# Performance work log

Hardware: AMD Instinct MI355X
Metric: run time of the kernel (lower is better)

The kernel has to match this reference:

```python
import jax, jax.numpy as jnp
import numpy as np

HIDDEN = 512
TEMPERATURE = float(np.sqrt(HIDDEN))  # scaled-dot temperature
BATCH = 64


def _build_weights(attn_weight, N, K):
    """Vectorized version of get_attn_weight: (S,S,H) with S = N*K+1.
    Regions: 0=same_sample, 1=same_class, 2=diff_class, 3=support->query,
    4=query->support, 5=query->query. Replicates the torch overwrite order."""
    S = N * K + 1
    NK = N * K
    i = jnp.arange(S)[:, None]
    j = jnp.arange(S)[None, :]
    idx = jnp.full((S, S), 2, dtype=jnp.int32)                      # w_diff_class
    idx = jnp.where((i // K) == (j // K), 1, idx)                   # w_same_class
    idx = jnp.where((i < NK) & (j == NK), 3, idx)                   # w_stoquery
    idx = jnp.where(i == j, 0, idx)                                 # w_same_sample (diag)
    idx = jnp.where((i == NK) & (j < NK), 4, idx)                   # w_querytos
    idx = jnp.where((i == NK) & (j == NK), 5, idx)                  # w_query
    return attn_weight[idx]  # (S, S, H)


def setup_inputs() -> dict:
    key = jax.random.key(0)
    kq, kk, kv, kw = jax.random.split(key, 4)
    N, K = 10, 10
    S = N * K + 1  # 101
    q = jax.random.normal(kq, (BATCH, S, HIDDEN), dtype=jnp.float32)
    k = jax.random.normal(kk, (BATCH, S, HIDDEN), dtype=jnp.float32)
    v = jax.random.normal(kv, (BATCH, S, HIDDEN), dtype=jnp.float32)
    bound = float(np.sqrt(6 / 2))
    attn_weight = jax.random.uniform(kw, (6, HIDDEN), dtype=jnp.float32,
                                     minval=-bound, maxval=bound)
    return {"q": q, "k": k, "v": v, "attn_weight": attn_weight, "N": N, "K": K}


def reference(q, k, v, attn_weight, N, K):
    # attn[b,i,j] = softmax_j(q.k^T / temperature)
    scores = jnp.einsum("bih,bjh->bij", q, k) / TEMPERATURE
    attn = jax.nn.softmax(scores, axis=2)  # dropout p=0 (eval) -> identity
    weights = _build_weights(attn_weight, N, K)  # (S,S,H)
    # out[b,i,h] = sum_j attn[b,i,j] * weights[i,j,h] * v[b,j,h]
    out = jnp.einsum("bij,ijh,bjh->bih", attn, weights, v)
    return out, attn
```

## Files before the change

### kernel.cpp

```cpp
#include <hip/hip_runtime.h>
#include <math.h>
#include <stdint.h>

#define BATCH 64
#define SEQ   101
#define HID   512
#define NKQ   100
#define KCLS  10
#define INV_TEMP 0.04419417382415922f
#define SPAD  128

typedef short bf16x8 __attribute__((ext_vector_type(8)));
typedef float f32x4  __attribute__((ext_vector_type(4)));

__device__ inline void split_bf16(float x, short& hi, short& lo) {
    uint32_t u = __builtin_bit_cast(uint32_t, x);
    hi = (short)(u >> 16);
    float hf = __builtin_bit_cast(float, u & 0xFFFF0000u);
    float l  = x - hf;
    lo = (short)(__builtin_bit_cast(uint32_t, l) >> 16);
}

__global__ __launch_bounds__(512, 4)
void fused_attn(const float* __restrict__ q, const float* __restrict__ k,
                const float* __restrict__ v, const float* __restrict__ aw,
                float* __restrict__ out, float* __restrict__ attn) {
    __shared__ float sc[16][132];
    __shared__ short ah_s[16][136];
    __shared__ short al_s[16][136];
    __shared__ short mh_s[16][136];

    const int b   = blockIdx.x & 63;
    const int i0  = (blockIdx.x >> 6) * 16;
    const int tid = threadIdx.x;
    const int wv  = tid >> 6, lane = tid & 63;
    const int m   = lane & 15;
    const int kq  = (lane >> 4) * 8;
    const int rq  = (lane >> 4) * 4;

    const float* qb = q + (size_t)b * SEQ * HID;
    const float* kb = k + (size_t)b * SEQ * HID;
    const float* vb = v + (size_t)b * SEQ * HID;

    {
        const int j0w = wv * 16;
        const int qrow = i0 + m;
        const int krow = j0w + m;
        f32x4 acc = {};
        for (int ks = 0; ks < HID; ks += 32) {
            float x[8];
            bf16x8 qh, ql, kh, kl;
            if (qrow < SEQ) {
                float4 u0 = *(const float4*)(qb + (size_t)qrow * HID + ks + kq);
                float4 u1 = *(const float4*)(qb + (size_t)qrow * HID + ks + kq + 4);
                x[0]=u0.x; x[1]=u0.y; x[2]=u0.z; x[3]=u0.w;
                x[4]=u1.x; x[5]=u1.y; x[6]=u1.z; x[7]=u1.w;
            } else {
                #pragma unroll
                for (int e = 0; e < 8; ++e) x[e] = 0.f;
            }
            #pragma unroll
            for (int e = 0; e < 8; ++e) { short h,l; split_bf16(x[e],h,l); qh[e]=h; ql[e]=l; }
            if (krow < SEQ) {
                float4 u0 = *(const float4*)(kb + (size_t)krow * HID + ks + kq);
                float4 u1 = *(const float4*)(kb + (size_t)krow * HID + ks + kq + 4);
                x[0]=u0.x; x[1]=u0.y; x[2]=u0.z; x[3]=u0.w;
                x[4]=u1.x; x[5]=u1.y; x[6]=u1.z; x[7]=u1.w;
            } else {
                #pragma unroll
                for (int e = 0; e < 8; ++e) x[e] = 0.f;
            }
            #pragma unroll
            for (int e = 0; e < 8; ++e) { short h,l; split_bf16(x[e],h,l); kh[e]=h; kl[e]=l; }
            acc = __builtin_amdgcn_mfma_f32_16x16x32_bf16(qh, kh, acc, 0, 0, 0);
            acc = __builtin_amdgcn_mfma_f32_16x16x32_bf16(qh, kl, acc, 0, 0, 0);
            acc = __builtin_amdgcn_mfma_f32_16x16x32_bf16(ql, kh, acc, 0, 0, 0);
        }
        #pragma unroll
        for (int r = 0; r < 4; ++r)
            sc[rq + r][j0w + m] = acc[r];
    }
    __syncthreads();

    {
        const int row = tid >> 5, t32 = tid & 31;
        const int gi  = i0 + row;
        float mx = -1e30f;
        for (int j = t32; j < SEQ; j += 32) {
            float s = sc[row][j] * INV_TEMP;
            sc[row][j] = s;
            mx = fmaxf(mx, s);
        }
        #pragma unroll
        for (int off = 1; off < 32; off <<= 1) mx = fmaxf(mx, __shfl_xor(mx, off));
        float sum = 0.f;
        for (int j = t32; j < SEQ; j += 32) {
            float e = __expf(sc[row][j] - mx);
            sc[row][j] = e;
            sum += e;
        }
        #pragma unroll
        for (int off = 1; off < 32; off <<= 1) sum += __shfl_xor(sum, off);
        const float inv = 1.f / sum;
        const int ci = gi / KCLS;
        float* arow = attn + ((size_t)b * SEQ + gi) * SEQ;
        for (int j = t32; j < SEQ; j += 32) {
            float a = sc[row][j] * inv;
            sc[row][j] = a;
            if (gi < SEQ) arow[j] = a;
            short h, l; split_bf16(a, h, l);
            ah_s[row][j] = h; al_s[row][j] = l;
            mh_s[row][j] = ((j / KCLS) == ci) ? h : (short)0;
        }
        for (int j = SEQ + t32; j < 136; j += 32) {
            ah_s[row][j] = 0; al_s[row][j] = 0; mh_s[row][j] = 0;
        }
    }
    __syncthreads();

    const int hw = wv * 64;
    f32x4 T[4] = {}, U[4] = {};
    for (int ks = 0; ks < SPAD; ks += 32) {
        const bf16x8 Ah = *(const bf16x8*)&ah_s[m][ks + kq];
        const bf16x8 Al = *(const bf16x8*)&al_s[m][ks + kq];
        const bf16x8 Mh = *(const bf16x8*)&mh_s[m][ks + kq];
        #pragma unroll
        for (int ht = 0; ht < 4; ++ht) {
            const int h = hw + ht * 16 + m;
            float x[8];
            #pragma unroll
            for (int e = 0; e < 8; ++e) {
                const int j = ks + kq + e;
                x[e] = (j < SEQ) ? vb[(size_t)j * HID + h] : 0.f;
            }
            bf16x8 Bh, Bl;
            #pragma unroll
            for (int e = 0; e < 8; ++e) { short hh,ll; split_bf16(x[e],hh,ll); Bh[e]=hh; Bl[e]=ll; }
            T[ht] = __builtin_amdgcn_mfma_f32_16x16x32_bf16(Ah, Bh, T[ht], 0, 0, 0);
            T[ht] = __builtin_amdgcn_mfma_f32_16x16x32_bf16(Ah, Bl, T[ht], 0, 0, 0);
            T[ht] = __builtin_amdgcn_mfma_f32_16x16x32_bf16(Al, Bh, T[ht], 0, 0, 0);
            U[ht] = __builtin_amdgcn_mfma_f32_16x16x32_bf16(Mh, Bh, U[ht], 0, 0, 0);
        }
    }

    #pragma unroll
    for (int ht = 0; ht < 4; ++ht) {
        const int h = hw + ht * 16 + m;
        const float w0 = aw[0 * HID + h], w1 = aw[1 * HID + h], w2 = aw[2 * HID + h];
        const float w3 = aw[3 * HID + h], w4 = aw[4 * HID + h], w5 = aw[5 * HID + h];
        const float vN = vb[(size_t)NKQ * HID + h];
        #pragma unroll
        for (int r = 0; r < 4; ++r) {
            const int il = rq + r;
            const int i  = i0 + il;
            if (i >= SEQ) continue;
            const float t = T[ht][r], u = U[ht][r];
            const float aiN = sc[il][NKQ];
            float o;
            if (i < NKQ) {
                const float aii = sc[il][i];
                const float vi  = vb[(size_t)i * HID + h];
                o = w2 * t + (w1 - w2) * u + (w0 - w1) * aii * vi + (w3 - w2) * aiN * vN;
            } else {
                o = w4 * t + (w5 - w4) * aiN * vN;
            }
            out[((size_t)b * SEQ + i) * HID + h] = o;
        }
    }
}

extern "C" void kernel_launch(void* const* d_in, const int* in_sizes, int n_in,
                              void* d_out, int out_size, void* d_ws, size_t ws_size,
                              hipStream_t stream) {
    const float* q  = (const float*)d_in[0];
    const float* k  = (const float*)d_in[1];
    const float* v  = (const float*)d_in[2];
    const float* aw = (const float*)d_in[3];
    float* out  = (float*)d_out;
    float* attn = out + (size_t)BATCH * SEQ * HID;

    fused_attn<<<dim3(448), dim3(512), 0, stream>>>(q, k, v, aw, out, attn);
}
```

Before: 121.0 us.

## Precompute bf16 hi/lo splits in prep kernel and split hidden dim across blocks

New measurement: 185.2 us. 53.1% more time.

```diff
diff --git a/kernel.cpp b/kernel.cpp
--- a/kernel.cpp
+++ b/kernel.cpp
@@ -8,10 +8,12 @@
 #define NKQ   100
 #define KCLS  10
 #define INV_TEMP 0.04419417382415922f
-#define SPAD  128
 
 typedef short bf16x8 __attribute__((ext_vector_type(8)));
 typedef float f32x4  __attribute__((ext_vector_type(4)));
+
+#define QK_PLANE ((size_t)BATCH * SEQ * HID)
+#define VT_PLANE ((size_t)BATCH * HID * 128)
 
 __device__ inline void split_bf16(float x, short& hi, short& lo) {
     uint32_t u = __builtin_bit_cast(uint32_t, x);
@@ -21,60 +23,97 @@
     lo = (short)(__builtin_bit_cast(uint32_t, l) >> 16);
 }
 
+__global__ __launch_bounds__(256)
+void prep_bf16(const float* __restrict__ q, const float* __restrict__ k,
+               const float* __restrict__ v,
+               short* __restrict__ qh, short* __restrict__ ql,
+               short* __restrict__ kh, short* __restrict__ kl,
+               short* __restrict__ vh, short* __restrict__ vl) {
+    const int tid = threadIdx.x;
+    if (blockIdx.x < 256) {
+        __shared__ float tile[SEQ][132];
+        const int b = blockIdx.x & 63, hc = (blockIdx.x >> 6) * 128;
+        const float* vb = v + (size_t)b * SEQ * HID + hc;
+        for (int f = tid; f < SEQ * 32; f += 256) {
+            int r = f >> 5, c = (f & 31) << 2;
+            *(float4*)&tile[r][c] = *(const float4*)(vb + (size_t)r * HID + c);
+        }
+        __syncthreads();
+        const int hl = tid >> 1;
+        const int j0 = (tid & 1) * 64;
+        const size_t ro = ((size_t)b * HID + hc + hl) * 128 + j0;
+        for (int jj = 0; jj < 64; jj += 4) {
+            short4 hv, lv;
+            int j = j0 + jj;
+            split_bf16(j + 0 < SEQ ? tile[j + 0][hl] : 0.f, hv.x, lv.x);
+            split_bf16(j + 1 < SEQ ? tile[j + 1][hl] : 0.f, hv.y, lv.y);
+            split_bf16(j + 2 < SEQ ? tile[j + 2][hl] : 0.f, hv.z, lv.z);
+            split_bf16(j + 3 < SEQ ? tile[j + 3][hl] : 0.f, hv.w, lv.w);
+            *(short4*)(vh + ro + jj) = hv;
+            *(short4*)(vl + ro + jj) = lv;
+        }
+    } else {
+        const size_t per = QK_PLANE / 4;
+        for (size_t f = (size_t)(blockIdx.x - 256) * 256 + tid;
+             f < 2 * per; f += (size_t)512 * 256) {
+            size_t e = f;
+            const float* src; short *dh, *dl;
+            if (e < per) { src = q; dh = qh; dl = ql; }
+            else         { e -= per; src = k; dh = kh; dl = kl; }
+            float4 x = ((const float4*)src)[e];
+            short4 hv, lv;
+            split_bf16(x.x, hv.x, lv.x);
+            split_bf16(x.y, hv.y, lv.y);
+            split_bf16(x.z, hv.z, lv.z);
+            split_bf16(x.w, hv.w, lv.w);
+            *(short4*)(dh + e * 4) = hv;
+            *(short4*)(dl + e * 4) = lv;
+        }
+    }
+}
+
 __global__ __launch_bounds__(512, 4)
-void fused_attn(const float* __restrict__ q, const float* __restrict__ k,
-                const float* __restrict__ v, const float* __restrict__ aw,
+void fused_attn(const float* __restrict__ v, const float* __restrict__ aw,
+                const short* __restrict__ qh, const short* __restrict__ ql,
+                const short* __restrict__ kh, const short* __restrict__ kl,
+                const short* __restrict__ vh, const short* __restrict__ vl,
                 float* __restrict__ out, float* __restrict__ attn) {
     __shared__ float sc[16][132];
     __shared__ short ah_s[16][136];
     __shared__ short al_s[16][136];
     __shared__ short mh_s[16][136];
 
-    const int b   = blockIdx.x & 63;
-    const int i0  = (blockIdx.x >> 6) * 16;
+    const int id  = blockIdx.x;
+    const int b   = id & 63;
+    const int rr  = id >> 6;
+    const int it  = rr % 7, hg = rr / 7;
+    const int i0  = it * 16;
     const int tid = threadIdx.x;
     const int wv  = tid >> 6, lane = tid & 63;
     const int m   = lane & 15;
     const int kq  = (lane >> 4) * 8;
     const int rq  = (lane >> 4) * 4;
 
-    const float* qb = q + (size_t)b * SEQ * HID;
-    const float* kb = k + (size_t)b * SEQ * HID;
     const float* vb = v + (size_t)b * SEQ * HID;
 
     {
         const int j0w = wv * 16;
-        const int qrow = i0 + m;
-        const int krow = j0w + m;
+        int qrow = i0 + m;  if (qrow > NKQ) qrow = NKQ;
+        int krow = j0w + m; if (krow > NKQ) krow = NKQ;
+        const short* qhr = qh + ((size_t)b * SEQ + qrow) * HID + kq;
+        const short* qlr = ql + ((size_t)b * SEQ + qrow) * HID + kq;
+        const short* khr = kh + ((size_t)b * SEQ + krow) * HID + kq;
+        const short* klr = kl + ((size_t)b * SEQ + krow) * HID + kq;
         f32x4 acc = {};
+        #pragma unroll 4
         for (int ks = 0; ks < HID; ks += 32) {
-            float x[8];
-            bf16x8 qh, ql, kh, kl;
-            if (qrow < SEQ) {
-                float4 u0 = *(const float4*)(qb + (size_t)qrow * HID + ks + kq);
-                float4 u1 = *(const float4*)(qb + (size_t)qrow * HID + ks + kq + 4);
-                x[0]=u0.x; x[1]=u0.y; x[2]=u0.z; x[3]=u0.w;
-                x[4]=u1.x; x[5]=u1.y; x[6]=u1.z; x[7]=u1.w;
-            } else {
-                #pragma unroll
-                for (int e = 0; e < 8; ++e) x[e] = 0.f;
-            }
-            #pragma unroll
-            for (int e = 0; e < 8; ++e) { short h,l; split_bf16(x[e],h,l); qh[e]=h; ql[e]=l; }
-            if (krow < SEQ) {
-                float4 u0 = *(const float4*)(kb + (size_t)krow * HID + ks + kq);
-                float4 u1 = *(const float4*)(kb + (size_t)krow * HID + ks + kq + 4);
-                x[0]=u0.x; x[1]=u0.y; x[2]=u0.z; x[3]=u0.w;
-                x[4]=u1.x; x[5]=u1.y; x[6]=u1.z; x[7]=u1.w;
-            } else {
-                #pragma unroll
-                for (int e = 0; e < 8; ++e) x[e] = 0.f;
-            }
-            #pragma unroll
-            for (int e = 0; e < 8; ++e) { short h,l; split_bf16(x[e],h,l); kh[e]=h; kl[e]=l; }
-            acc = __builtin_amdgcn_mfma_f32_16x16x32_bf16(qh, kh, acc, 0, 0, 0);
-            acc = __builtin_amdgcn_mfma_f32_16x16x32_bf16(qh, kl, acc, 0, 0, 0);
-            acc = __builtin_amdgcn_mfma_f32_16x16x32_bf16(ql, kh, acc, 0, 0, 0);
+            bf16x8 aH = *(const bf16x8*)(qhr + ks);
+            bf16x8 aL = *(const bf16x8*)(qlr + ks);
+            bf16x8 bH = *(const bf16x8*)(khr + ks);
+            bf16x8 bL = *(const bf16x8*)(klr + ks);
+            acc = __builtin_amdgcn_mfma_f32_16x16x32_bf16(aH, bH, acc, 0, 0, 0);
+            acc = __builtin_amdgcn_mfma_f32_16x16x32_bf16(aH, bL, acc, 0, 0, 0);
+            acc = __builtin_amdgcn_mfma_f32_16x16x32_bf16(aL, bH, acc, 0, 0, 0);
         }
         #pragma unroll
         for (int r = 0; r < 4; ++r)
@@ -107,7 +146,7 @@
         for (int j = t32; j < SEQ; j += 32) {
             float a = sc[row][j] * inv;
             sc[row][j] = a;
-            if (gi < SEQ) arow[j] = a;
+            if (hg == 0 && gi < SEQ) arow[j] = a;
             short h, l; split_bf16(a, h, l);
             ah_s[row][j] = h; al_s[row][j] = l;
             mh_s[row][j] = ((j / KCLS) == ci) ? h : (short)0;
@@ -118,24 +157,19 @@
     }
     __syncthreads();
 
-    const int hw = wv * 64;
-    f32x4 T[4] = {}, U[4] = {};
-    for (int ks = 0; ks < SPAD; ks += 32) {
+    const int hb = hg * 256 + wv * 32;
+    f32x4 T[2] = {}, U[2] = {};
+    #pragma unroll
+    for (int ks = 0; ks < 128; ks += 32) {
         const bf16x8 Ah = *(const bf16x8*)&ah_s[m][ks + kq];
         const bf16x8 Al = *(const bf16x8*)&al_s[m][ks + kq];
         const bf16x8 Mh = *(const bf16x8*)&mh_s[m][ks + kq];
         #pragma unroll
-        for (int ht = 0; ht < 4; ++ht) {
-            const int h = hw + ht * 16 + m;
-            float x[8];
-            #pragma unroll
-            for (int e = 0; e < 8; ++e) {
-                const int j = ks + kq + e;
-                x[e] = (j < SEQ) ? vb[(size_t)j * HID + h] : 0.f;
-            }
-            bf16x8 Bh, Bl;
-            #pragma unroll
-            for (int e = 0; e < 8; ++e) { short hh,ll; split_bf16(x[e],hh,ll); Bh[e]=hh; Bl[e]=ll; }
+        for (int ht = 0; ht < 2; ++ht) {
+            const int h = hb + ht * 16 + m;
+            const size_t vo = ((size_t)b * HID + h) * 128 + ks + kq;
+            const bf16x8 Bh = *(const bf16x8*)(vh + vo);
+            const bf16x8 Bl = *(const bf16x8*)(vl + vo);
             T[ht] = __builtin_amdgcn_mfma_f32_16x16x32_bf16(Ah, Bh, T[ht], 0, 0, 0);
             T[ht] = __builtin_amdgcn_mfma_f32_16x16x32_bf16(Ah, Bl, T[ht], 0, 0, 0);
             T[ht] = __builtin_amdgcn_mfma_f32_16x16x32_bf16(Al, Bh, T[ht], 0, 0, 0);
@@ -144,8 +178,8 @@
     }
 
     #pragma unroll
-    for (int ht = 0; ht < 4; ++ht) {
-        const int h = hw + ht * 16 + m;
+    for (int ht = 0; ht < 2; ++ht) {
+        const int h = hb + ht * 16 + m;
         const float w0 = aw[0 * HID + h], w1 = aw[1 * HID + h], w2 = aw[2 * HID + h];
         const float w3 = aw[3 * HID + h], w4 = aw[4 * HID + h], w5 = aw[5 * HID + h];
         const float vN = vb[(size_t)NKQ * HID + h];
@@ -179,5 +213,14 @@
     float* out  = (float*)d_out;
     float* attn = out + (size_t)BATCH * SEQ * HID;
 
-    fused_attn<<<dim3(448), dim3(512), 0, stream>>>(q, k, v, aw, out, attn);
-}
+    short* qh = (short*)d_ws;
+    short* ql = qh + QK_PLANE;
+    short* kh = ql + QK_PLANE;
+    short* kl = kh + QK_PLANE;
+    short* vh = kl + QK_PLANE;
+    short* vl = vh + VT_PLANE;
+
+    prep_bf16<<<dim3(768), dim3(256), 0, stream>>>(q, k, v, qh, ql, kh, kl, vh, vl);
+    fused_attn<<<dim3(896), dim3(512), 0, stream>>>(v, aw, qh, ql, kh, kl, vh, vl,
+                                                    out, attn);
+}
```

## Split fused attention into QK-softmax and PV kernels with LDS-staged V

Applied to the files above, without the earlier changes.

Measured after the change: 126.5 us. 4.6% more time.

```diff
diff --git a/kernel.cpp b/kernel.cpp
--- a/kernel.cpp
+++ b/kernel.cpp
@@ -8,7 +8,6 @@
 #define NKQ   100
 #define KCLS  10
 #define INV_TEMP 0.04419417382415922f
-#define SPAD  128
 
 typedef short bf16x8 __attribute__((ext_vector_type(8)));
 typedef float f32x4  __attribute__((ext_vector_type(4)));
@@ -22,14 +21,9 @@
 }
 
 __global__ __launch_bounds__(512, 4)
-void fused_attn(const float* __restrict__ q, const float* __restrict__ k,
-                const float* __restrict__ v, const float* __restrict__ aw,
-                float* __restrict__ out, float* __restrict__ attn) {
+void qk_softmax(const float* __restrict__ q, const float* __restrict__ k,
+                float* __restrict__ attn, float* __restrict__ apad) {
     __shared__ float sc[16][132];
-    __shared__ short ah_s[16][136];
-    __shared__ short al_s[16][136];
-    __shared__ short mh_s[16][136];
-
     const int b   = blockIdx.x & 63;
     const int i0  = (blockIdx.x >> 6) * 16;
     const int tid = threadIdx.x;
@@ -40,41 +34,30 @@
 
     const float* qb = q + (size_t)b * SEQ * HID;
     const float* kb = k + (size_t)b * SEQ * HID;
-    const float* vb = v + (size_t)b * SEQ * HID;
 
     {
         const int j0w = wv * 16;
-        const int qrow = i0 + m;
-        const int krow = j0w + m;
+        int qrow = i0 + m;  if (qrow > NKQ) qrow = NKQ;
+        int krow = j0w + m; if (krow > NKQ) krow = NKQ;
+        const float* qr = qb + (size_t)qrow * HID + kq;
+        const float* kr = kb + (size_t)krow * HID + kq;
         f32x4 acc = {};
+        #pragma unroll 4
         for (int ks = 0; ks < HID; ks += 32) {
-            float x[8];
-            bf16x8 qh, ql, kh, kl;
-            if (qrow < SEQ) {
-                float4 u0 = *(const float4*)(qb + (size_t)qrow * HID + ks + kq);
-                float4 u1 = *(const float4*)(qb + (size_t)qrow * HID + ks + kq + 4);
-                x[0]=u0.x; x[1]=u0.y; x[2]=u0.z; x[3]=u0.w;
-                x[4]=u1.x; x[5]=u1.y; x[6]=u1.z; x[7]=u1.w;
-            } else {
-                #pragma unroll
-                for (int e = 0; e < 8; ++e) x[e] = 0.f;
-            }
-            #pragma unroll
-            for (int e = 0; e < 8; ++e) { short h,l; split_bf16(x[e],h,l); qh[e]=h; ql[e]=l; }
-            if (krow < SEQ) {
-                float4 u0 = *(const float4*)(kb + (size_t)krow * HID + ks + kq);
-                float4 u1 = *(const float4*)(kb + (size_t)krow * HID + ks + kq + 4);
-                x[0]=u0.x; x[1]=u0.y; x[2]=u0.z; x[3]=u0.w;
-                x[4]=u1.x; x[5]=u1.y; x[6]=u1.z; x[7]=u1.w;
-            } else {
-                #pragma unroll
-                for (int e = 0; e < 8; ++e) x[e] = 0.f;
-            }
-            #pragma unroll
-            for (int e = 0; e < 8; ++e) { short h,l; split_bf16(x[e],h,l); kh[e]=h; kl[e]=l; }
-            acc = __builtin_amdgcn_mfma_f32_16x16x32_bf16(qh, kh, acc, 0, 0, 0);
-            acc = __builtin_amdgcn_mfma_f32_16x16x32_bf16(qh, kl, acc, 0, 0, 0);
-            acc = __builtin_amdgcn_mfma_f32_16x16x32_bf16(ql, kh, acc, 0, 0, 0);
+            float4 a0 = *(const float4*)(qr + ks);
+            float4 a1 = *(const float4*)(qr + ks + 4);
+            float4 b0 = *(const float4*)(kr + ks);
+            float4 b1 = *(const float4*)(kr + ks + 4);
+            float xa[8] = {a0.x,a0.y,a0.z,a0.w,a1.x,a1.y,a1.z,a1.w};
+            float xb[8] = {b0.x,b0.y,b0.z,b0.w,b1.x,b1.y,b1.z,b1.w};
+            bf16x8 aH, aL, bH, bL;
+            #pragma unroll
+            for (int e = 0; e < 8; ++e) { short h,l; split_bf16(xa[e],h,l); aH[e]=h; aL[e]=l; }
+            #pragma unroll
+            for (int e = 0; e < 8; ++e) { short h,l; split_bf16(xb[e],h,l); bH[e]=h; bL[e]=l; }
+            acc = __builtin_amdgcn_mfma_f32_16x16x32_bf16(aH, bH, acc, 0, 0, 0);
+            acc = __builtin_amdgcn_mfma_f32_16x16x32_bf16(aH, bL, acc, 0, 0, 0);
+            acc = __builtin_amdgcn_mfma_f32_16x16x32_bf16(aL, bH, acc, 0, 0, 0);
         }
         #pragma unroll
         for (int r = 0; r < 4; ++r)
@@ -102,69 +85,107 @@
         #pragma unroll
         for (int off = 1; off < 32; off <<= 1) sum += __shfl_xor(sum, off);
         const float inv = 1.f / sum;
-        const int ci = gi / KCLS;
-        float* arow = attn + ((size_t)b * SEQ + gi) * SEQ;
-        for (int j = t32; j < SEQ; j += 32) {
-            float a = sc[row][j] * inv;
-            sc[row][j] = a;
-            if (gi < SEQ) arow[j] = a;
-            short h, l; split_bf16(a, h, l);
-            ah_s[row][j] = h; al_s[row][j] = l;
-            mh_s[row][j] = ((j / KCLS) == ci) ? h : (short)0;
-        }
-        for (int j = SEQ + t32; j < 136; j += 32) {
-            ah_s[row][j] = 0; al_s[row][j] = 0; mh_s[row][j] = 0;
-        }
+        if (gi < SEQ) {
+            float* arow = attn + ((size_t)b * SEQ + gi) * SEQ;
+            float* prow = apad + ((size_t)b * SEQ + gi) * 128;
+            for (int j = t32; j < SEQ; j += 32) {
+                float a = sc[row][j] * inv;
+                arow[j] = a;
+                prow[j] = a;
+            }
+            for (int j = SEQ + t32; j < 128; j += 32) prow[j] = 0.f;
+        }
+    }
+}
+
+#define VR 36
+#define VT 144
+
+__global__ __launch_bounds__(512, 6)
+void pv_out(const float* __restrict__ v, const float* __restrict__ aw,
+            const float* __restrict__ apad, float* __restrict__ out) {
+    __shared__ float vraw[SEQ][VR];
+    __shared__ short vth[32][VT];
+    __shared__ short vtl[32][VT];
+    const int b   = blockIdx.x & 63;
+    const int h0  = (blockIdx.x >> 6) * 32;
+    const int tid = threadIdx.x;
+    const int wv  = tid >> 6, lane = tid & 63;
+    const int m   = lane & 15;
+    const int kq  = (lane >> 4) * 8;
+    const int rq  = (lane >> 4) * 4;
+
+    const float* vb = v + (size_t)b * SEQ * HID + h0;
+    for (int f = tid; f < SEQ * 8; f += 512) {
+        int r = f >> 3, c = (f & 7) << 2;
+        *(float4*)&vraw[r][c] = *(const float4*)(vb + (size_t)r * HID + c);
     }
     __syncthreads();
-
-    const int hw = wv * 64;
-    f32x4 T[4] = {}, U[4] = {};
-    for (int ks = 0; ks < SPAD; ks += 32) {
-        const bf16x8 Ah = *(const bf16x8*)&ah_s[m][ks + kq];
-        const bf16x8 Al = *(const bf16x8*)&al_s[m][ks + kq];
-        const bf16x8 Mh = *(const bf16x8*)&mh_s[m][ks + kq];
-        #pragma unroll
-        for (int ht = 0; ht < 4; ++ht) {
-            const int h = hw + ht * 16 + m;
-            float x[8];
+    for (int it2 = tid; it2 < 32 * 36; it2 += 512) {
+        int h = it2 & 31, j = (it2 >> 5) << 2;
+        short4 hv, lv;
+        split_bf16(j + 0 < SEQ ? vraw[j + 0][h] : 0.f, hv.x, lv.x);
+        split_bf16(j + 1 < SEQ ? vraw[j + 1][h] : 0.f, hv.y, lv.y);
+        split_bf16(j + 2 < SEQ ? vraw[j + 2][h] : 0.f, hv.z, lv.z);
+        split_bf16(j + 3 < SEQ ? vraw[j + 3][h] : 0.f, hv.w, lv.w);
+        *(short4*)&vth[h][j] = hv;
+        *(short4*)&vtl[h][j] = lv;
+    }
+    __syncthreads();
+
+    if (wv < 7) {
+        const int i0 = wv * 16;
+        int ai = i0 + m; if (ai > NKQ) ai = NKQ;
+        const int ci = ai / KCLS;
+        const float* ar = apad + ((size_t)b * SEQ + ai) * 128 + kq;
+        f32x4 T[2] = {}, U[2] = {};
+        #pragma unroll
+        for (int ks = 0; ks < 4; ++ks) {
+            float4 u0 = *(const float4*)(ar + ks * 32);
+            float4 u1 = *(const float4*)(ar + ks * 32 + 4);
+            float x[8] = {u0.x,u0.y,u0.z,u0.w,u1.x,u1.y,u1.z,u1.w};
+            bf16x8 Ah, Al, Mh;
             #pragma unroll
             for (int e = 0; e < 8; ++e) {
-                const int j = ks + kq + e;
-                x[e] = (j < SEQ) ? vb[(size_t)j * HID + h] : 0.f;
-            }
-            bf16x8 Bh, Bl;
-            #pragma unroll
-            for (int e = 0; e < 8; ++e) { short hh,ll; split_bf16(x[e],hh,ll); Bh[e]=hh; Bl[e]=ll; }
-            T[ht] = __builtin_amdgcn_mfma_f32_16x16x32_bf16(Ah, Bh, T[ht], 0, 0, 0);
-            T[ht] = __builtin_amdgcn_mfma_f32_16x16x32_bf16(Ah, Bl, T[ht], 0, 0, 0);
-            T[ht] = __builtin_amdgcn_mfma_f32_16x16x32_bf16(Al, Bh, T[ht], 0, 0, 0);
-            U[ht] = __builtin_amdgcn_mfma_f32_16x16x32_bf16(Mh, Bh, U[ht], 0, 0, 0);
-        }
-    }
-
-    #pragma unroll
-    for (int ht = 0; ht < 4; ++ht) {
-        const int h = hw + ht * 16 + m;
-        const float w0 = aw[0 * HID + h], w1 = aw[1 * HID + h], w2 = aw[2 * HID + h];
-        const float w3 = aw[3 * HID + h], w4 = aw[4 * HID + h], w5 = aw[5 * HID + h];
-        const float vN = vb[(size_t)NKQ * HID + h];
-        #pragma unroll
-        for (int r = 0; r < 4; ++r) {
-            const int il = rq + r;
-            const int i  = i0 + il;
-            if (i >= SEQ) continue;
-            const float t = T[ht][r], u = U[ht][r];
-            const float aiN = sc[il][NKQ];
-            float o;
-            if (i < NKQ) {
-                const float aii = sc[il][i];
-                const float vi  = vb[(size_t)i * HID + h];
-                o = w2 * t + (w1 - w2) * u + (w0 - w1) * aii * vi + (w3 - w2) * aiN * vN;
-            } else {
-                o = w4 * t + (w5 - w4) * aiN * vN;
-            }
-            out[((size_t)b * SEQ + i) * HID + h] = o;
+                short h, l; split_bf16(x[e], h, l);
+                Ah[e] = h; Al[e] = l;
+                const int j = ks * 32 + kq + e;
+                Mh[e] = ((j / KCLS) == ci) ? h : (short)0;
+            }
+            #pragma unroll
+            for (int ht = 0; ht < 2; ++ht) {
+                const bf16x8 Bh = *(const bf16x8*)&vth[ht * 16 + m][ks * 32 + kq];
+                const bf16x8 Bl = *(const bf16x8*)&vtl[ht * 16 + m][ks * 32 + kq];
+                T[ht] = __builtin_amdgcn_mfma_f32_16x16x32_bf16(Ah, Bh, T[ht], 0, 0, 0);
+                T[ht] = __builtin_amdgcn_mfma_f32_16x16x32_bf16(Ah, Bl, T[ht], 0, 0, 0);
+                T[ht] = __builtin_amdgcn_mfma_f32_16x16x32_bf16(Al, Bh, T[ht], 0, 0, 0);
+                U[ht] = __builtin_amdgcn_mfma_f32_16x16x32_bf16(Mh, Bh, U[ht], 0, 0, 0);
+            }
+        }
+        const float* ap = apad + (size_t)b * SEQ * 128;
+        #pragma unroll
+        for (int ht = 0; ht < 2; ++ht) {
+            const int hl = ht * 16 + m;
+            const int h  = h0 + hl;
+            const float w0 = aw[0 * HID + h], w1 = aw[1 * HID + h], w2 = aw[2 * HID + h];
+            const float w3 = aw[3 * HID + h], w4 = aw[4 * HID + h], w5 = aw[5 * HID + h];
+            const float vN = vraw[NKQ][hl];
+            #pragma unroll
+            for (int r = 0; r < 4; ++r) {
+                const int i = i0 + rq + r;
+                if (i >= SEQ) continue;
+                const float t = T[ht][r], u = U[ht][r];
+                const float aiN = ap[(size_t)i * 128 + NKQ];
+                float o;
+                if (i < NKQ) {
+                    const float aii = ap[(size_t)i * 128 + i];
+                    const float vi  = vraw[i][hl];
+                    o = w2 * t + (w1 - w2) * u + (w0 - w1) * aii * vi + (w3 - w2) * aiN * vN;
+                } else {
+                    o = w4 * t + (w5 - w4) * aiN * vN;
+                }
+                out[((size_t)b * SEQ + i) * HID + h] = o;
+            }
         }
     }
 }
@@ -178,6 +199,8 @@
     const float* aw = (const float*)d_in[3];
     float* out  = (float*)d_out;
     float* attn = out + (size_t)BATCH * SEQ * HID;
-
-    fused_attn<<<dim3(448), dim3(512), 0, stream>>>(q, k, v, aw, out, attn);
-}
+    float* apad = (float*)d_ws;
+
+    qk_softmax<<<dim3(448), dim3(512), 0, stream>>>(q, k, attn, apad);
+    pv_out<<<dim3(1024), dim3(512), 0, stream>>>(v, aw, apad, out);
+}
```

## Stage Q/K and transposed V tiles in shared memory for MFMA phases

Applied to the files above, without the earlier changes.

New measurement: 138.1 us. 1.14x slower.

```diff
diff --git a/kernel.cpp b/kernel.cpp
--- a/kernel.cpp
+++ b/kernel.cpp
@@ -8,7 +8,6 @@
 #define NKQ   100
 #define KCLS  10
 #define INV_TEMP 0.04419417382415922f
-#define SPAD  128
 
 typedef short bf16x8 __attribute__((ext_vector_type(8)));
 typedef float f32x4  __attribute__((ext_vector_type(4)));
@@ -20,6 +19,13 @@
     float l  = x - hf;
     lo = (short)(__builtin_bit_cast(uint32_t, l) >> 16);
 }
+__device__ inline short rtn_bf16(float x) {
+    uint32_t u = __builtin_bit_cast(uint32_t, x);
+    return (short)((u + 0x7FFFu + ((u >> 16) & 1u)) >> 16);
+}
+
+#define KST 72
+#define VT  152
 
 __global__ __launch_bounds__(512, 4)
 void fused_attn(const float* __restrict__ q, const float* __restrict__ k,
@@ -29,6 +35,12 @@
     __shared__ short ah_s[16][136];
     __shared__ short al_s[16][136];
     __shared__ short mh_s[16][136];
+    __shared__ __align__(16) char pool[38912];
+    short (*khi)[KST] = (short(*)[KST])pool;
+    short (*qhi)[KST] = (short(*)[KST])(pool + 18432);
+    short (*qlo)[KST] = (short(*)[KST])(pool + 20736);
+    short (*vth)[VT]  = (short(*)[VT])pool;
+    short (*vtl)[VT]  = (short(*)[VT])(pool + 19456);
 
     const int b   = blockIdx.x & 63;
     const int i0  = (blockIdx.x >> 6) * 16;
@@ -37,49 +49,52 @@
     const int m   = lane & 15;
     const int kq  = (lane >> 4) * 8;
     const int rq  = (lane >> 4) * 4;
+    const int j0w = wv * 16;
 
     const float* qb = q + (size_t)b * SEQ * HID;
     const float* kb = k + (size_t)b * SEQ * HID;
     const float* vb = v + (size_t)b * SEQ * HID;
 
-    {
-        const int j0w = wv * 16;
-        const int qrow = i0 + m;
-        const int krow = j0w + m;
-        f32x4 acc = {};
-        for (int ks = 0; ks < HID; ks += 32) {
-            float x[8];
-            bf16x8 qh, ql, kh, kl;
-            if (qrow < SEQ) {
-                float4 u0 = *(const float4*)(qb + (size_t)qrow * HID + ks + kq);
-                float4 u1 = *(const float4*)(qb + (size_t)qrow * HID + ks + kq + 4);
-                x[0]=u0.x; x[1]=u0.y; x[2]=u0.z; x[3]=u0.w;
-                x[4]=u1.x; x[5]=u1.y; x[6]=u1.z; x[7]=u1.w;
-            } else {
-                #pragma unroll
-                for (int e = 0; e < 8; ++e) x[e] = 0.f;
-            }
-            #pragma unroll
-            for (int e = 0; e < 8; ++e) { short h,l; split_bf16(x[e],h,l); qh[e]=h; ql[e]=l; }
-            if (krow < SEQ) {
-                float4 u0 = *(const float4*)(kb + (size_t)krow * HID + ks + kq);
-                float4 u1 = *(const float4*)(kb + (size_t)krow * HID + ks + kq + 4);
-                x[0]=u0.x; x[1]=u0.y; x[2]=u0.z; x[3]=u0.w;
-                x[4]=u1.x; x[5]=u1.y; x[6]=u1.z; x[7]=u1.w;
-            } else {
-                #pragma unroll
-                for (int e = 0; e < 8; ++e) x[e] = 0.f;
-            }
-            #pragma unroll
-            for (int e = 0; e < 8; ++e) { short h,l; split_bf16(x[e],h,l); kh[e]=h; kl[e]=l; }
-            acc = __builtin_amdgcn_mfma_f32_16x16x32_bf16(qh, kh, acc, 0, 0, 0);
-            acc = __builtin_amdgcn_mfma_f32_16x16x32_bf16(qh, kl, acc, 0, 0, 0);
-            acc = __builtin_amdgcn_mfma_f32_16x16x32_bf16(ql, kh, acc, 0, 0, 0);
-        }
-        #pragma unroll
-        for (int r = 0; r < 4; ++r)
-            sc[rq + r][j0w + m] = acc[r];
-    }
+    f32x4 acc = {};
+    for (int kc = 0; kc < HID; kc += 64) {
+        #pragma unroll
+        for (int s = 0; s < 4; ++s) {
+            const int f = tid + s * 512;
+            const int r = f >> 4, c = (f & 15) << 2;
+            float4 x = make_float4(0.f, 0.f, 0.f, 0.f);
+            if (r < SEQ) x = *(const float4*)(kb + (size_t)r * HID + kc + c);
+            short4 hv;
+            hv.x = rtn_bf16(x.x); hv.y = rtn_bf16(x.y);
+            hv.z = rtn_bf16(x.z); hv.w = rtn_bf16(x.w);
+            *(short4*)&khi[r][c] = hv;
+        }
+        if (tid < 256) {
+            const int r = tid >> 4, c = (tid & 15) << 2;
+            const int gi = i0 + r;
+            float4 x = make_float4(0.f, 0.f, 0.f, 0.f);
+            if (gi < SEQ) x = *(const float4*)(qb + (size_t)gi * HID + kc + c);
+            short4 hv, lv;
+            split_bf16(x.x, hv.x, lv.x);
+            split_bf16(x.y, hv.y, lv.y);
+            split_bf16(x.z, hv.z, lv.z);
+            split_bf16(x.w, hv.w, lv.w);
+            *(short4*)&qhi[r][c] = hv;
+            *(short4*)&qlo[r][c] = lv;
+        }
+        __syncthreads();
+        #pragma unroll
+        for (int ks = 0; ks < 64; ks += 32) {
+            const bf16x8 qH = *(const bf16x8*)&qhi[m][ks + kq];
+            const bf16x8 qL = *(const bf16x8*)&qlo[m][ks + kq];
+            const bf16x8 kH = *(const bf16x8*)&khi[j0w + m][ks + kq];
+            acc = __builtin_amdgcn_mfma_f32_16x16x32_bf16(qH, kH, acc, 0, 0, 0);
+            acc = __builtin_amdgcn_mfma_f32_16x16x32_bf16(qL, kH, acc, 0, 0, 0);
+        }
+        __syncthreads();
+    }
+    #pragma unroll
+    for (int r = 0; r < 4; ++r)
+        sc[rq + r][j0w + m] = acc[r];
     __syncthreads();
 
     {
@@ -118,54 +133,67 @@
     }
     __syncthreads();
 
-    const int hw = wv * 64;
-    f32x4 T[4] = {}, U[4] = {};
-    for (int ks = 0; ks < SPAD; ks += 32) {
-        const bf16x8 Ah = *(const bf16x8*)&ah_s[m][ks + kq];
-        const bf16x8 Al = *(const bf16x8*)&al_s[m][ks + kq];
-        const bf16x8 Mh = *(const bf16x8*)&mh_s[m][ks + kq];
-        #pragma unroll
-        for (int ht = 0; ht < 4; ++ht) {
-            const int h = hw + ht * 16 + m;
-            float x[8];
+    bf16x8 Ah[4], Al[4], Mh[4];
+    if (wv < 4) {
+        #pragma unroll
+        for (int s = 0; s < 4; ++s) {
+            Ah[s] = *(const bf16x8*)&ah_s[m][s * 32 + kq];
+            Al[s] = *(const bf16x8*)&al_s[m][s * 32 + kq];
+            Mh[s] = *(const bf16x8*)&mh_s[m][s * 32 + kq];
+        }
+    }
+    for (int hc = 0; hc < HID; hc += 64) {
+        #pragma unroll
+        for (int s = 0; s < 4; ++s) {
+            const int f = tid + s * 512;
+            const int j = f >> 4;
+            const int c = (f & 15) << 2;
+            float4 x = make_float4(0.f, 0.f, 0.f, 0.f);
+            if (j < SEQ) x = *(const float4*)(vb + (size_t)j * HID + hc + c);
+            short h0, l0, h1, l1, h2, l2, h3, l3;
+            split_bf16(x.x, h0, l0);
+            split_bf16(x.y, h1, l1);
+            split_bf16(x.z, h2, l2);
+            split_bf16(x.w, h3, l3);
+            vth[c + 0][j] = h0; vtl[c + 0][j] = l0;
+            vth[c + 1][j] = h1; vtl[c + 1][j] = l1;
+            vth[c + 2][j] = h2; vtl[c + 2][j] = l2;
+            vth[c + 3][j] = h3; vtl[c + 3][j] = l3;
+        }
+        __syncthreads();
+        if (wv < 4) {
+            f32x4 T = {}, U = {};
             #pragma unroll
-            for (int e = 0; e < 8; ++e) {
-                const int j = ks + kq + e;
-                x[e] = (j < SEQ) ? vb[(size_t)j * HID + h] : 0.f;
+            for (int s = 0; s < 4; ++s) {
+                const bf16x8 Bh = *(const bf16x8*)&vth[wv * 16 + m][s * 32 + kq];
+                const bf16x8 Bl = *(const bf16x8*)&vtl[wv * 16 + m][s * 32 + kq];
+                T = __builtin_amdgcn_mfma_f32_16x16x32_bf16(Ah[s], Bh, T, 0, 0, 0);
+                T = __builtin_amdgcn_mfma_f32_16x16x32_bf16(Ah[s], Bl, T, 0, 0, 0);
+                T = __builtin_amdgcn_mfma_f32_16x16x32_bf16(Al[s], Bh, T, 0, 0, 0);
+                U = __builtin_amdgcn_mfma_f32_16x16x32_bf16(Mh[s], Bh, U, 0, 0, 0);
             }
-            bf16x8 Bh, Bl;
+            const int h = hc + wv * 16 + m;
+            const float w0 = aw[0 * HID + h], w1 = aw[1 * HID + h], w2 = aw[2 * HID + h];
+            const float w3 = aw[3 * HID + h], w4 = aw[4 * HID + h], w5 = aw[5 * HID + h];
+            const float vN = vb[(size_t)NKQ * HID + h];
             #pragma unroll
-            for (int e = 0; e < 8; ++e) { short hh,ll; split_bf16(x[e],hh,ll); Bh[e]=hh; Bl[e]=ll; }
-            T[ht] = __builtin_amdgcn_mfma_f32_16x16x32_bf16(Ah, Bh, T[ht], 0, 0, 0);
-            T[ht] = __builtin_amdgcn_mfma_f32_16x16x32_bf16(Ah, Bl, T[ht], 0, 0, 0);
-            T[ht] = __builtin_amdgcn_mfma_f32_16x16x32_bf16(Al, Bh, T[ht], 0, 0, 0);
-            U[ht] = __builtin_amdgcn_mfma_f32_16x16x32_bf16(Mh, Bh, U[ht], 0, 0, 0);
-        }
-    }
-
-    #pragma unroll
-    for (int ht = 0; ht < 4; ++ht) {
-        const int h = hw + ht * 16 + m;
-        const float w0 = aw[0 * HID + h], w1 = aw[1 * HID + h], w2 = aw[2 * HID + h];
-        const float w3 = aw[3 * HID + h], w4 = aw[4 * HID + h], w5 = aw[5 * HID + h];
-        const float vN = vb[(size_t)NKQ * HID + h];
-        #pragma unroll
-        for (int r = 0; r < 4; ++r) {
-            const int il = rq + r;
-            const int i  = i0 + il;
-            if (i >= SEQ) continue;
-            const float t = T[ht][r], u = U[ht][r];
-            const float aiN = sc[il][NKQ];
-            float o;
-            if (i < NKQ) {
-                const float aii = sc[il][i];
-                const float vi  = vb[(size_t)i * HID + h];
-                o = w2 * t + (w1 - w2) * u + (w0 - w1) * aii * vi + (w3 - w2) * aiN * vN;
-            } else {
-                o = w4 * t + (w5 - w4) * aiN * vN;
+            for (int r = 0; r < 4; ++r) {
+                const int il = rq + r;
+                const int i  = i0 + il;
+                if (i >= SEQ) continue;
+                const float aiN = sc[il][NKQ];
+                float o;
+                if (i < NKQ) {
+                    const float aii = sc[il][i];
+                    const float vi  = vb[(size_t)i * HID + h];
+                    o = w2 * T[r] + (w1 - w2) * U[r] + (w0 - w1) * aii * vi + (w3 - w2) * aiN * vN;
+                } else {
+                    o = w4 * T[r] + (w5 - w4) * aiN * vN;
+                }
+                out[((size_t)b * SEQ + i) * HID + h] = o;
             }
-            out[((size_t)b * SEQ + i) * HID + h] = o;
-        }
+        }
+        __syncthreads();
     }
 }
 
```
